# Performance work log

Hardware: AMD Instinct MI355X
Metric: run time of the kernel (lower is better)

The kernel has to match this reference:

```python
import jax, jax.numpy as jnp
import numpy as np

N_NODES = 100000
IN_CH, HIDDEN, OUT_CH = 128, 64, 40
N_EDGES = 1600000


def gcn_conv(x, row, col, W, b, num_nodes):
    """PyG GCNConv: x' = D^-1/2 (A+I) D^-1/2 (x W) + b, self-loops already in row/col."""
    h = x @ W  # [N, out]
    deg = jax.ops.segment_sum(jnp.ones_like(col, dtype=h.dtype), col, num_segments=num_nodes)
    dinv = jnp.where(deg > 0, jax.lax.rsqrt(deg), 0.0)  # [N]
    norm = dinv[row] * dinv[col]  # [E+N]
    msg = h[row] * norm[:, None]  # gather + scale
    out = jax.ops.segment_sum(msg, col, num_segments=num_nodes)  # scatter-add to targets
    return out + b


def setup_inputs() -> dict:
    key = jax.random.key(0)
    k = jax.random.split(key, 6)
    x = jax.random.normal(k[0], (N_NODES, IN_CH), dtype=jnp.float32)
    ei = jax.random.randint(k[1], (2, N_EDGES), 0, N_NODES, dtype=jnp.int64)
    # Glorot-style init for linear weights, zeros for biases (PyG defaults)
    W1 = jax.random.normal(k[2], (IN_CH, HIDDEN), dtype=jnp.float32) / np.sqrt(IN_CH)
    b1 = jnp.zeros((HIDDEN,), dtype=jnp.float32)
    W2 = jax.random.normal(k[3], (HIDDEN, OUT_CH), dtype=jnp.float32) / np.sqrt(HIDDEN)
    b2 = jnp.zeros((OUT_CH,), dtype=jnp.float32)
    return {"x": x, "ei": ei, "W1": W1, "b1": b1, "W2": W2, "b2": b2}


def reference(x, ei, W1, b1, W2, b2):
    num_nodes = x.shape[0]
    loop = jnp.arange(num_nodes, dtype=ei.dtype)
    row = jnp.concatenate([ei[0], loop])  # sources + self-loops
    col = jnp.concatenate([ei[1], loop])  # targets + self-loops
    h = jax.nn.relu(gcn_conv(x, row, col, W1, b1, num_nodes))
    # dropout(p=0.5) is identity in eval mode (deterministic reference)
    return gcn_conv(h, row, col, W2, b2, num_nodes)
```

## Files before the change

kernel.cpp:

```cpp
#include <hip/hip_runtime.h>
#include <hip/hip_bf16.h>
#include <math.h>

#define IN_CH 128
#define HID 64
#define OUT_CH 40
#define NBUCK 1024
#define NBSHIFT 10
#define CAP2 3125
#define CAPL 2560

typedef const __hip_bfloat16* bf16p;
typedef __attribute__((ext_vector_type(8))) short bf16x8;
typedef __attribute__((ext_vector_type(4))) float f32x4;
typedef __attribute__((ext_vector_type(8))) float f32x8;

__device__ __forceinline__ f32x8 cvt8(bf16x8 v) {
    f32x8 o;
    #pragma unroll
    for (int j = 0; j < 8; ++j) {
        unsigned int bits = ((unsigned int)(unsigned short)v[j]) << 16;
        o[j] = __uint_as_float(bits);
    }
    return o;
}

__device__ __forceinline__ bf16x8 pack8(f32x8 v) {
    bf16x8 o;
    #pragma unroll
    for (int j = 0; j < 8; ++j) {
        __hip_bfloat16 b = __float2bfloat16(v[j]);
        o[j] = *reinterpret_cast<short*>(&b);
    }
    return o;
}

__device__ __forceinline__ int bucket_of(int c, int N, float invNB) {
    int b = (int)((float)c * invNB);
    long long cB = (long long)c << NBSHIFT;
    while ((long long)(b + 1) * N <= cB) ++b;
    while (b > 0 && (long long)b * N > cB) --b;
    return b;
}

__global__ __launch_bounds__(256) void k_detectconv(const void* x, const void* ei,
        int* flags, const void* W1, const void* b1, const void* W2, const void* b2,
        float* wf) {
    __shared__ int s_f32, s_hi;
    if (threadIdx.x == 0) { s_f32 = 0; s_hi = 0; }
    __syncthreads();
    const __hip_bfloat16* xb = (const __hip_bfloat16*)x;
    const int* ii = (const int*)ei;
    int lf = 0, lh = 0;
    for (int i = threadIdx.x; i < 4096; i += 256) {
        float f = __bfloat162float(xb[i]);
        if (!(fabsf(f) <= 1e4f)) lf = 1;
        lh |= ii[2 * i + 1];
    }
    if (lf) atomicOr(&s_f32, 1);
    if (lh) atomicOr(&s_hi, 1);
    __syncthreads();
    const int isF32 = s_f32 ? 1 : 0;
    if (threadIdx.x == 0) {
        flags[0] = isF32;
        flags[1] = (s_hi == 0) ? 1 : 0;
        flags[2] = 0;
    }
    for (int i = threadIdx.x; i < 10856; i += 256) {
        const void* src; int off;
        if (i < 8192)       { src = W1; off = i; }
        else if (i < 8256)  { src = b1; off = i - 8192; }
        else if (i < 10816) { src = W2; off = i - 8256; }
        else                { src = b2; off = i - 10816; }
        wf[i] = isF32 ? ((const float*)src)[off]
                      : __bfloat162float(((bf16p)src)[off]);
    }
}

__global__ __launch_bounds__(512) void k_bin2(const int* ei, const int* flags,
        int* bincnt2, long long* bins2, int E, int N, float invNB) {
    __shared__ int cnt[NBUCK], base[NBUCK];
    for (int i = threadIdx.x; i < NBUCK; i += 512) cnt[i] = 0;
    __syncthreads();
    const int i64 = flags[1];
    const int e0 = blockIdx.x * 4096;
    const int e1 = min(e0 + 4096, E);
    int e = e0 + threadIdx.x;
    for (; e + 3 * 512 < e1; e += 4 * 512) {
        int c0 = i64 ? ei[2 * (E + e)]        : ei[E + e];
        int c1 = i64 ? ei[2 * (E + e + 512)]  : ei[E + e + 512];
        int c2 = i64 ? ei[2 * (E + e + 1024)] : ei[E + e + 1024];
        int c3 = i64 ? ei[2 * (E + e + 1536)] : ei[E + e + 1536];
        atomicAdd(&cnt[bucket_of(c0, N, invNB)], 1);
        atomicAdd(&cnt[bucket_of(c1, N, invNB)], 1);
        atomicAdd(&cnt[bucket_of(c2, N, invNB)], 1);
        atomicAdd(&cnt[bucket_of(c3, N, invNB)], 1);
    }
    for (; e < e1; e += 512) {
        int c = i64 ? ei[2 * (E + e)] : ei[E + e];
        atomicAdd(&cnt[bucket_of(c, N, invNB)], 1);
    }
    __syncthreads();
    for (int i = threadIdx.x; i < NBUCK; i += 512) {
        int v = cnt[i];
        base[i] = v ? atomicAdd(&bincnt2[i], v) : 0;
        cnt[i] = 0;
    }
    __syncthreads();
    for (e = e0 + threadIdx.x; e < e1; e += 512) {
        int r, c;
        if (i64) { r = ei[2 * e]; c = ei[2 * (E + e)]; }
        else     { r = ei[e];     c = ei[E + e]; }
        int b = bucket_of(c, N, invNB);
        int slot = base[b] + atomicAdd(&cnt[b], 1);
        if (slot < CAP2)
            bins2[(size_t)b * CAP2 + slot] = ((long long)r << 32) | (unsigned int)c;
    }
}

__global__ __launch_bounds__(256) void k_csr(const long long* bins2, const int* bincnt2,
        int* rowstart, float* dinv, int* erow, int N) {
    __shared__ long long rc[CAPL];
    __shared__ int sdeg[256], lcur[256], red[256];
    const int s = blockIdx.x;
    const int tid = threadIdx.x;
    int part = 0;
    for (int j = tid; j < s; j += 256) part += min(bincnt2[j], CAPL);
    red[tid] = part;
    __syncthreads();
    for (int o = 128; o > 0; o >>= 1) {
        if (tid < o) red[tid] += red[tid + o];
        __syncthreads();
    }
    const int gb = red[0];
    const int nlo = (int)(((long long)s * N + NBUCK - 1) >> NBSHIFT);
    const int nhi = (int)(((long long)(s + 1) * N + NBUCK - 1) >> NBSHIFT);
    const int width = nhi - nlo;
    const int cnt = min(bincnt2[s], CAPL);

    for (int i = tid; i < cnt; i += 256) rc[i] = bins2[(size_t)s * CAP2 + i];
    sdeg[tid] = 0;
    __syncthreads();
    for (int i = tid; i < cnt; i += 256) {
        int j = (int)(rc[i] & 0xffffffffLL) - nlo;
        if (j >= 0 && j < width) atomicAdd(&sdeg[j], 1);
    }
    __syncthreads();
    int my = sdeg[tid];
    __syncthreads();
    for (int off = 1; off < 256; off <<= 1) {
        int t = (tid >= off) ? sdeg[tid - off] : 0;
        __syncthreads();
        sdeg[tid] += t;
        __syncthreads();
    }
    int excl = sdeg[tid] - my;
    lcur[tid] = excl;
    if (tid < width) {
        rowstart[nlo + tid] = gb + excl;
        dinv[nlo + tid] = rsqrtf((float)my + 1.0f);
    }
    if (s == NBUCK - 1 && tid == 0) rowstart[N] = gb + cnt;
    __syncthreads();
    for (int i = tid; i < cnt; i += 256) {
        long long v = rc[i];
        int j = (int)(v & 0xffffffffLL) - nlo;
        if (j >= 0 && j < width) {
            int pos = atomicAdd(&lcur[j], 1);
            erow[gb + pos] = (int)(v >> 32);
        }
    }
}

__global__ __launch_bounds__(256) void k_gemm1_mfma(const void* x, const float* W1f,
        __hip_bfloat16* h1b, const int* flags, int N) {
    __shared__ __align__(16) unsigned short wT[HID][IN_CH];
    for (int i = threadIdx.x; i < IN_CH * HID; i += 256) {
        int k = i >> 6, c = i & 63;
        __hip_bfloat16 b = __float2bfloat16(W1f[i]);
        wT[c][k] = *reinterpret_cast<unsigned short*>(&b);
    }
    __syncthreads();

    const int isF32 = flags[0];
    const int lane = threadIdx.x & 63;
    const int wid  = threadIdx.x >> 6;
    const int r = lane & 15;
    const int g = lane >> 4;

    bf16x8 bfr[4][4];
    #pragma unroll
    for (int nt = 0; nt < 4; ++nt)
        #pragma unroll
        for (int ks = 0; ks < 4; ++ks)
            bfr[nt][ks] = *(const bf16x8*)&wT[nt * 16 + r][ks * 32 + g * 8];

    const int tiles = (N + 15) >> 4;
    for (int t = blockIdx.x * 4 + wid; t < tiles; t += gridDim.x * 4) {
        const int row0 = t * 16;
        int arow = row0 + r; if (arow >= N) arow = N - 1;
        bf16x8 afr[4];
        if (!isF32) {
            const unsigned short* xr = (const unsigned short*)x + (size_t)arow * IN_CH;
            #pragma unroll
            for (int ks = 0; ks < 4; ++ks)
                afr[ks] = *(const bf16x8*)&xr[ks * 32 + g * 8];
        } else {
            const float* xr = (const float*)x + (size_t)arow * IN_CH;
            #pragma unroll
            for (int ks = 0; ks < 4; ++ks) {
                #pragma unroll
                for (int j = 0; j < 8; ++j) {
                    __hip_bfloat16 b = __float2bfloat16(xr[ks * 32 + g * 8 + j]);
                    afr[ks][j] = *reinterpret_cast<short*>(&b);
                }
            }
        }
        f32x4 acc[4] = {};
        #pragma unroll
        for (int ks = 0; ks < 4; ++ks)
            #pragma unroll
            for (int nt = 0; nt < 4; ++nt)
                acc[nt] = __builtin_amdgcn_mfma_f32_16x16x32_bf16(afr[ks], bfr[nt][ks],
                                                                  acc[nt], 0, 0, 0);
        #pragma unroll
        for (int nt = 0; nt < 4; ++nt) {
            #pragma unroll
            for (int q = 0; q < 4; ++q) {
                int rr = row0 + g * 4 + q;
                if (rr < N)
                    h1b[(size_t)rr * HID + nt * 16 + r] = __float2bfloat16(acc[nt][q]);
            }
        }
    }
}

__global__ __launch_bounds__(256) void k_agg1(const int* rowstart, const int* erow,
        const __hip_bfloat16* h1b, const float* dinv, const float* b1f,
        __hip_bfloat16* g, int N) {
    const int lane = threadIdx.x & 63;
    const int sub = lane >> 3;
    const int co  = lane & 7;
    const f32x4 b1a = *(const f32x4*)&b1f[co * 8];
    const f32x4 b1b = *(const f32x4*)&b1f[co * 8 + 4];
    const int wstride = (gridDim.x * 256) >> 6;
    for (int w = (blockIdx.x * 256 + threadIdx.x) >> 6; w < N; w += wstride) {
        int s0 = __builtin_amdgcn_readfirstlane(rowstart[w]);
        int s1 = __builtin_amdgcn_readfirstlane(rowstart[w + 1]);
        float d = dinv[w];
        bf16x8 sv = *(const bf16x8*)&h1b[(size_t)w * HID + co * 8];
        f32x8 acc = {};
        int i = s0 + sub;
        for (; i + 8 < s1; i += 16) {
            int r0 = erow[i], r1 = erow[i + 8];
            float n0 = dinv[r0] * d, n1 = dinv[r1] * d;
            f32x8 v0 = cvt8(*(const bf16x8*)&h1b[(size_t)r0 * HID + co * 8]);
            f32x8 v1 = cvt8(*(const bf16x8*)&h1b[(size_t)r1 * HID + co * 8]);
            #pragma unroll
            for (int j = 0; j < 8; ++j) {
                acc[j] = fmaf(v0[j], n0, acc[j]);
                acc[j] = fmaf(v1[j], n1, acc[j]);
            }
        }
        if (i < s1) {
            int r0 = erow[i];
            float n0 = dinv[r0] * d;
            f32x8 v0 = cvt8(*(const bf16x8*)&h1b[(size_t)r0 * HID + co * 8]);
            #pragma unroll
            for (int j = 0; j < 8; ++j) acc[j] = fmaf(v0[j], n0, acc[j]);
        }
        #pragma unroll
        for (int j = 0; j < 8; ++j) {
            acc[j] += __shfl_xor(acc[j], 8);
            acc[j] += __shfl_xor(acc[j], 16);
            acc[j] += __shfl_xor(acc[j], 32);
        }
        if (sub == 0) {
            float dd = d * d;
            f32x8 sf = cvt8(sv);
            f32x8 gv;
            #pragma unroll
            for (int j = 0; j < 4; ++j) {
                gv[j]     = fmaxf(fmaf(sf[j], dd, acc[j]) + b1a[j], 0.f);
                gv[j + 4] = fmaxf(fmaf(sf[j + 4], dd, acc[j + 4]) + b1b[j], 0.f);
            }
            *(bf16x8*)&g[(size_t)w * HID + co * 8] = pack8(gv);
        }
    }
}

__global__ __launch_bounds__(256) void k_agg2s(const int* rowstart, const int* erow,
        const __hip_bfloat16* g, const float* dinv, __hip_bfloat16* sbuf, int N) {
    const int lane = threadIdx.x & 63;
    const int sub = lane >> 3;
    const int co  = lane & 7;
    const int wstride = (gridDim.x * 256) >> 6;
    for (int w = (blockIdx.x * 256 + threadIdx.x) >> 6; w < N; w += wstride) {
        int s0 = __builtin_amdgcn_readfirstlane(rowstart[w]);
        int s1 = __builtin_amdgcn_readfirstlane(rowstart[w + 1]);
        float d = dinv[w];
        bf16x8 sv = *(const bf16x8*)&g[(size_t)w * HID + co * 8];
        f32x8 acc = {};
        int i = s0 + sub;
        for (; i + 8 < s1; i += 16) {
            int r0 = erow[i], r1 = erow[i + 8];
            float n0 = dinv[r0] * d, n1 = dinv[r1] * d;
            f32x8 v0 = cvt8(*(const bf16x8*)&g[(size_t)r0 * HID + co * 8]);
            f32x8 v1 = cvt8(*(const bf16x8*)&g[(size_t)r1 * HID + co * 8]);
            #pragma unroll
            for (int j = 0; j < 8; ++j) {
                acc[j] = fmaf(v0[j], n0, acc[j]);
                acc[j] = fmaf(v1[j], n1, acc[j]);
            }
        }
        if (i < s1) {
            int r0 = erow[i];
            float n0 = dinv[r0] * d;
            f32x8 v0 = cvt8(*(const bf16x8*)&g[(size_t)r0 * HID + co * 8]);
            #pragma unroll
            for (int j = 0; j < 8; ++j) acc[j] = fmaf(v0[j], n0, acc[j]);
        }
        #pragma unroll
        for (int j = 0; j < 8; ++j) {
            acc[j] += __shfl_xor(acc[j], 8);
            acc[j] += __shfl_xor(acc[j], 16);
            acc[j] += __shfl_xor(acc[j], 32);
        }
        if (sub == 0) {
            float dd = d * d;
            f32x8 sf = cvt8(sv);
            f32x8 ov;
            #pragma unroll
            for (int j = 0; j < 8; ++j) ov[j] = fmaf(sf[j], dd, acc[j]);
            *(bf16x8*)&sbuf[(size_t)w * HID + co * 8] = pack8(ov);
        }
    }
}

__global__ __launch_bounds__(256) void k_gemm2_mfma(const __hip_bfloat16* sbuf,
        const float* W2f, const float* b2f, float* out, int N) {
    __shared__ __align__(16) unsigned short w2T[48][HID];
    for (int i = threadIdx.x; i < 48 * HID; i += 256) {
        int c = i >> 6, k = i & 63;
        float v = (c < OUT_CH) ? W2f[k * OUT_CH + c] : 0.f;
        __hip_bfloat16 b = __float2bfloat16(v);
        w2T[c][k] = *reinterpret_cast<unsigned short*>(&b);
    }
    __syncthreads();

    const int lane = threadIdx.x & 63;
    const int wid  = threadIdx.x >> 6;
    const int r = lane & 15;
    const int gq = lane >> 4;

    bf16x8 bfr[3][2];
    #pragma unroll
    for (int nt = 0; nt < 3; ++nt)
        #pragma unroll
        for (int ks = 0; ks < 2; ++ks)
            bfr[nt][ks] = *(const bf16x8*)&w2T[nt * 16 + r][ks * 32 + gq * 8];
    float b2v[3];
    #pragma unroll
    for (int nt = 0; nt < 3; ++nt)
        b2v[nt] = (nt * 16 + r < OUT_CH) ? b2f[nt * 16 + r] : 0.f;

    const int tiles = (N + 15) >> 4;
    for (int t = blockIdx.x * 4 + wid; t < tiles; t += gridDim.x * 4) {
        const int row0 = t * 16;
        int arow = row0 + r; if (arow >= N) arow = N - 1;
        const unsigned short* sr = (const unsigned short*)sbuf + (size_t)arow * HID;
        bf16x8 afr[2];
        afr[0] = *(const bf16x8*)&sr[gq * 8];
        afr[1] = *(const bf16x8*)&sr[32 + gq * 8];
        f32x4 acc[3] = {};
        #pragma unroll
        for (int ks = 0; ks < 2; ++ks)
            #pragma unroll
            for (int nt = 0; nt < 3; ++nt)
                acc[nt] = __builtin_amdgcn_mfma_f32_16x16x32_bf16(afr[ks], bfr[nt][ks],
                                                                  acc[nt], 0, 0, 0);
        #pragma unroll
        for (int nt = 0; nt < 3; ++nt) {
            int c = nt * 16 + r;
            #pragma unroll
            for (int q = 0; q < 4; ++q) {
                int rr = row0 + gq * 4 + q;
                if (rr < N && c < OUT_CH)
                    out[(size_t)rr * OUT_CH + c] = acc[nt][q] + b2v[nt];
            }
        }
    }
}

extern "C" void kernel_launch(void* const* d_in, const int* in_sizes, int n_in,
                              void* d_out, int out_size, void* d_ws, size_t ws_size,
                              hipStream_t stream) {
    const void* x  = d_in[0];
    const void* ei = d_in[1];
    const void* W1 = d_in[2];
    const void* b1 = d_in[3];
    const void* W2 = d_in[4];
    const void* b2 = d_in[5];
    const int N = in_sizes[0] / IN_CH;
    const int E = in_sizes[1] / 2;
    const int* eii = (const int*)ei;

    float* ws = (float*)d_ws;
    size_t off = 16;
    int*   flags    = (int*)ws;
    int*   bincnt2  = (int*)ws + off;            off += NBUCK;
    float* dinv     = ws + off;                  off += N;
    float* wf       = ws + off;                  off += 10880;
    int*   rowstart = (int*)ws + off;            off += N + 1;
    off = (off + 255) & ~(size_t)255;
    int*   erow     = (int*)ws + off;            off += E;
    off = (off + 255) & ~(size_t)255;
    __hip_bfloat16* h1b = (__hip_bfloat16*)(ws + off);     off += (size_t)N * HID / 2;
    __hip_bfloat16* g   = (__hip_bfloat16*)(ws + off);     off += (size_t)N * HID / 2;
    __hip_bfloat16* sbuf = h1b;
    long long* bins2 = (long long*)h1b;

    hipMemsetAsync(bincnt2, 0, NBUCK * sizeof(int), stream);

    k_detectconv<<<1, 256, 0, stream>>>(x, ei, flags, W1, b1, W2, b2, wf);

    float invNB = (float)NBUCK / (float)N;
    int nbin = (E + 4095) / 4096;
    k_bin2<<<nbin, 512, 0, stream>>>(eii, flags, bincnt2, bins2, E, N, invNB);
    k_csr<<<NBUCK, 256, 0, stream>>>(bins2, bincnt2, rowstart, dinv, erow, N);

    int tiles = (N + 15) / 16;
    int g1 = (tiles + 7) / 8;
    k_gemm1_mfma<<<g1, 256, 0, stream>>>(x, wf, h1b, flags, N);

    k_agg1<<<4096, 256, 0, stream>>>(rowstart, erow, h1b, dinv, wf + 8192, g, N);
    k_agg2s<<<4096, 256, 0, stream>>>(rowstart, erow, g, dinv, sbuf, N);
    k_gemm2_mfma<<<g1, 256, 0, stream>>>(sbuf, wf + 8256, wf + 10816, (float*)d_out, N);
}
```

Baseline: 269.6 us.

## Merge edge binning and first GEMM into one launch; fold memset into detect kernel

Edge binning and the first MFMA GEMM become a single kernel whose blocks branch on blockIdx, so the two independent stages can run concurrently on the GPU. The bins buffer gets its own workspace region instead of aliasing h1b, and the bucket-counter memset moves into the detect kernel, removing one launch. The f32 input path now uses vectorized 16-byte loads. The cost is a larger workspace footprint and a block size of 256 instead of 512 for the binning blocks.

Result: slower. 279.4 us (+3.6%).

```diff
diff --git a/kernel.cpp b/kernel.cpp
--- a/kernel.cpp
+++ b/kernel.cpp
@@ -45,7 +45,7 @@
 
 __global__ __launch_bounds__(256) void k_detectconv(const void* x, const void* ei,
         int* flags, const void* W1, const void* b1, const void* W2, const void* b2,
-        float* wf) {
+        float* wf, int* bincnt2) {
     __shared__ int s_f32, s_hi;
     if (threadIdx.x == 0) { s_f32 = 0; s_hi = 0; }
     __syncthreads();
@@ -59,6 +59,7 @@
     }
     if (lf) atomicOr(&s_f32, 1);
     if (lh) atomicOr(&s_hi, 1);
+    for (int i = threadIdx.x; i < NBUCK; i += 256) bincnt2[i] = 0;
     __syncthreads();
     const int isF32 = s_f32 ? 1 : 0;
     if (threadIdx.x == 0) {
@@ -77,44 +78,116 @@
     }
 }
 
-__global__ __launch_bounds__(512) void k_bin2(const int* ei, const int* flags,
-        int* bincnt2, long long* bins2, int E, int N, float invNB) {
-    __shared__ int cnt[NBUCK], base[NBUCK];
-    for (int i = threadIdx.x; i < NBUCK; i += 512) cnt[i] = 0;
-    __syncthreads();
-    const int i64 = flags[1];
-    const int e0 = blockIdx.x * 4096;
-    const int e1 = min(e0 + 4096, E);
-    int e = e0 + threadIdx.x;
-    for (; e + 3 * 512 < e1; e += 4 * 512) {
-        int c0 = i64 ? ei[2 * (E + e)]        : ei[E + e];
-        int c1 = i64 ? ei[2 * (E + e + 512)]  : ei[E + e + 512];
-        int c2 = i64 ? ei[2 * (E + e + 1024)] : ei[E + e + 1024];
-        int c3 = i64 ? ei[2 * (E + e + 1536)] : ei[E + e + 1536];
-        atomicAdd(&cnt[bucket_of(c0, N, invNB)], 1);
-        atomicAdd(&cnt[bucket_of(c1, N, invNB)], 1);
-        atomicAdd(&cnt[bucket_of(c2, N, invNB)], 1);
-        atomicAdd(&cnt[bucket_of(c3, N, invNB)], 1);
-    }
-    for (; e < e1; e += 512) {
-        int c = i64 ? ei[2 * (E + e)] : ei[E + e];
-        atomicAdd(&cnt[bucket_of(c, N, invNB)], 1);
-    }
-    __syncthreads();
-    for (int i = threadIdx.x; i < NBUCK; i += 512) {
-        int v = cnt[i];
-        base[i] = v ? atomicAdd(&bincnt2[i], v) : 0;
-        cnt[i] = 0;
-    }
-    __syncthreads();
-    for (e = e0 + threadIdx.x; e < e1; e += 512) {
-        int r, c;
-        if (i64) { r = ei[2 * e]; c = ei[2 * (E + e)]; }
-        else     { r = ei[e];     c = ei[E + e]; }
-        int b = bucket_of(c, N, invNB);
-        int slot = base[b] + atomicAdd(&cnt[b], 1);
-        if (slot < CAP2)
-            bins2[(size_t)b * CAP2 + slot] = ((long long)r << 32) | (unsigned int)c;
+__global__ __launch_bounds__(256) void k_bin_gemm1(const int* ei, const int* flags,
+        int* bincnt2, long long* bins2, int E, int N, float invNB, int nbin,
+        const void* x, const float* W1f, __hip_bfloat16* h1b, int g1) {
+    __shared__ __align__(16) unsigned char smem[16384];
+
+    if (blockIdx.x < nbin) {
+        int* cnt  = (int*)smem;
+        int* base = (int*)(smem + 4096);
+        for (int i = threadIdx.x; i < NBUCK; i += 256) cnt[i] = 0;
+        __syncthreads();
+        const int i64 = flags[1];
+        const int e0 = blockIdx.x * 4096;
+        const int e1 = min(e0 + 4096, E);
+        int e = e0 + threadIdx.x;
+        for (; e + 3 * 256 < e1; e += 4 * 256) {
+            int c0 = i64 ? ei[2 * (E + e)]       : ei[E + e];
+            int c1 = i64 ? ei[2 * (E + e + 256)] : ei[E + e + 256];
+            int c2 = i64 ? ei[2 * (E + e + 512)] : ei[E + e + 512];
+            int c3 = i64 ? ei[2 * (E + e + 768)] : ei[E + e + 768];
+            atomicAdd(&cnt[bucket_of(c0, N, invNB)], 1);
+            atomicAdd(&cnt[bucket_of(c1, N, invNB)], 1);
+            atomicAdd(&cnt[bucket_of(c2, N, invNB)], 1);
+            atomicAdd(&cnt[bucket_of(c3, N, invNB)], 1);
+        }
+        for (; e < e1; e += 256) {
+            int c = i64 ? ei[2 * (E + e)] : ei[E + e];
+            atomicAdd(&cnt[bucket_of(c, N, invNB)], 1);
+        }
+        __syncthreads();
+        for (int i = threadIdx.x; i < NBUCK; i += 256) {
+            int v = cnt[i];
+            base[i] = v ? atomicAdd(&bincnt2[i], v) : 0;
+            cnt[i] = 0;
+        }
+        __syncthreads();
+        for (e = e0 + threadIdx.x; e < e1; e += 256) {
+            int r, c;
+            if (i64) { r = ei[2 * e]; c = ei[2 * (E + e)]; }
+            else     { r = ei[e];     c = ei[E + e]; }
+            int b = bucket_of(c, N, invNB);
+            int slot = base[b] + atomicAdd(&cnt[b], 1);
+            if (slot < CAP2)
+                bins2[(size_t)b * CAP2 + slot] = ((long long)r << 32) | (unsigned int)c;
+        }
+        return;
+    }
+
+    unsigned short (*wT)[IN_CH] = (unsigned short(*)[IN_CH])smem;
+    for (int i = threadIdx.x; i < IN_CH * HID; i += 256) {
+        int k = i >> 6, c = i & 63;
+        __hip_bfloat16 b = __float2bfloat16(W1f[i]);
+        wT[c][k] = *reinterpret_cast<unsigned short*>(&b);
+    }
+    __syncthreads();
+
+    const int isF32 = flags[0];
+    const int lane = threadIdx.x & 63;
+    const int wid  = threadIdx.x >> 6;
+    const int r = lane & 15;
+    const int g = lane >> 4;
+    const int bb = blockIdx.x - nbin;
+
+    bf16x8 bfr[4][4];
+    #pragma unroll
+    for (int nt = 0; nt < 4; ++nt)
+        #pragma unroll
+        for (int ks = 0; ks < 4; ++ks)
+            bfr[nt][ks] = *(const bf16x8*)&wT[nt * 16 + r][ks * 32 + g * 8];
+
+    const int tiles = (N + 15) >> 4;
+    for (int t = bb * 4 + wid; t < tiles; t += g1 * 4) {
+        const int row0 = t * 16;
+        int arow = row0 + r; if (arow >= N) arow = N - 1;
+        bf16x8 afr[4];
+        if (!isF32) {
+            const unsigned short* xr = (const unsigned short*)x + (size_t)arow * IN_CH;
+            #pragma unroll
+            for (int ks = 0; ks < 4; ++ks)
+                afr[ks] = *(const bf16x8*)&xr[ks * 32 + g * 8];
+        } else {
+            const float* xr = (const float*)x + (size_t)arow * IN_CH;
+            #pragma unroll
+            for (int ks = 0; ks < 4; ++ks) {
+                f32x4 a0 = *(const f32x4*)&xr[ks * 32 + g * 8];
+                f32x4 a1 = *(const f32x4*)&xr[ks * 32 + g * 8 + 4];
+                #pragma unroll
+                for (int j = 0; j < 4; ++j) {
+                    __hip_bfloat16 b0 = __float2bfloat16(a0[j]);
+                    __hip_bfloat16 b1v = __float2bfloat16(a1[j]);
+                    afr[ks][j]     = *reinterpret_cast<short*>(&b0);
+                    afr[ks][j + 4] = *reinterpret_cast<short*>(&b1v);
+                }
+            }
+        }
+        f32x4 acc[4] = {};
+        #pragma unroll
+        for (int ks = 0; ks < 4; ++ks)
+            #pragma unroll
+            for (int nt = 0; nt < 4; ++nt)
+                acc[nt] = __builtin_amdgcn_mfma_f32_16x16x32_bf16(afr[ks], bfr[nt][ks],
+                                                                  acc[nt], 0, 0, 0);
+        #pragma unroll
+        for (int nt = 0; nt < 4; ++nt) {
+            #pragma unroll
+            for (int q = 0; q < 4; ++q) {
+                int rr = row0 + g * 4 + q;
+                if (rr < N)
+                    h1b[(size_t)rr * HID + nt * 16 + r] = __float2bfloat16(acc[nt][q]);
+            }
+        }
     }
 }
 
@@ -168,69 +241,6 @@
         if (j >= 0 && j < width) {
             int pos = atomicAdd(&lcur[j], 1);
             erow[gb + pos] = (int)(v >> 32);
-        }
-    }
-}
-
-__global__ __launch_bounds__(256) void k_gemm1_mfma(const void* x, const float* W1f,
-        __hip_bfloat16* h1b, const int* flags, int N) {
-    __shared__ __align__(16) unsigned short wT[HID][IN_CH];
-    for (int i = threadIdx.x; i < IN_CH * HID; i += 256) {
-        int k = i >> 6, c = i & 63;
-        __hip_bfloat16 b = __float2bfloat16(W1f[i]);
-        wT[c][k] = *reinterpret_cast<unsigned short*>(&b);
-    }
-    __syncthreads();
-
-    const int isF32 = flags[0];
-    const int lane = threadIdx.x & 63;
-    const int wid  = threadIdx.x >> 6;
-    const int r = lane & 15;
-    const int g = lane >> 4;
-
-    bf16x8 bfr[4][4];
-    #pragma unroll
-    for (int nt = 0; nt < 4; ++nt)
-        #pragma unroll
-        for (int ks = 0; ks < 4; ++ks)
-            bfr[nt][ks] = *(const bf16x8*)&wT[nt * 16 + r][ks * 32 + g * 8];
-
-    const int tiles = (N + 15) >> 4;
-    for (int t = blockIdx.x * 4 + wid; t < tiles; t += gridDim.x * 4) {
-        const int row0 = t * 16;
-        int arow = row0 + r; if (arow >= N) arow = N - 1;
-        bf16x8 afr[4];
-        if (!isF32) {
-            const unsigned short* xr = (const unsigned short*)x + (size_t)arow * IN_CH;
-            #pragma unroll
-            for (int ks = 0; ks < 4; ++ks)
-                afr[ks] = *(const bf16x8*)&xr[ks * 32 + g * 8];
-        } else {
-            const float* xr = (const float*)x + (size_t)arow * IN_CH;
-            #pragma unroll
-            for (int ks = 0; ks < 4; ++ks) {
-                #pragma unroll
-                for (int j = 0; j < 8; ++j) {
-                    __hip_bfloat16 b = __float2bfloat16(xr[ks * 32 + g * 8 + j]);
-                    afr[ks][j] = *reinterpret_cast<short*>(&b);
-                }
-            }
-        }
-        f32x4 acc[4] = {};
-        #pragma unroll
-        for (int ks = 0; ks < 4; ++ks)
-            #pragma unroll
-            for (int nt = 0; nt < 4; ++nt)
-                acc[nt] = __builtin_amdgcn_mfma_f32_16x16x32_bf16(afr[ks], bfr[nt][ks],
-                                                                  acc[nt], 0, 0, 0);
-        #pragma unroll
-        for (int nt = 0; nt < 4; ++nt) {
-            #pragma unroll
-            for (int q = 0; q < 4; ++q) {
-                int rr = row0 + g * 4 + q;
-                if (rr < N)
-                    h1b[(size_t)rr * HID + nt * 16 + r] = __float2bfloat16(acc[nt][q]);
-            }
         }
     }
 }
@@ -417,21 +427,19 @@
     off = (off + 255) & ~(size_t)255;
     __hip_bfloat16* h1b = (__hip_bfloat16*)(ws + off);     off += (size_t)N * HID / 2;
     __hip_bfloat16* g   = (__hip_bfloat16*)(ws + off);     off += (size_t)N * HID / 2;
+    off = (off + 255) & ~(size_t)255;
+    long long* bins2 = (long long*)(ws + off);   off += (size_t)NBUCK * CAP2 * 2;
     __hip_bfloat16* sbuf = h1b;
-    long long* bins2 = (long long*)h1b;
-
-    hipMemsetAsync(bincnt2, 0, NBUCK * sizeof(int), stream);
-
-    k_detectconv<<<1, 256, 0, stream>>>(x, ei, flags, W1, b1, W2, b2, wf);
+
+    k_detectconv<<<1, 256, 0, stream>>>(x, ei, flags, W1, b1, W2, b2, wf, bincnt2);
 
     float invNB = (float)NBUCK / (float)N;
     int nbin = (E + 4095) / 4096;
-    k_bin2<<<nbin, 512, 0, stream>>>(eii, flags, bincnt2, bins2, E, N, invNB);
-    k_csr<<<NBUCK, 256, 0, stream>>>(bins2, bincnt2, rowstart, dinv, erow, N);
-
     int tiles = (N + 15) / 16;
     int g1 = (tiles + 7) / 8;
-    k_gemm1_mfma<<<g1, 256, 0, stream>>>(x, wf, h1b, flags, N);
+    k_bin_gemm1<<<nbin + g1, 256, 0, stream>>>(eii, flags, bincnt2, bins2, E, N,
+                                               invNB, nbin, x, wf, h1b, g1);
+    k_csr<<<NBUCK, 256, 0, stream>>>(bins2, bincnt2, rowstart, dinv, erow, N);
 
     k_agg1<<<4096, 256, 0, stream>>>(rowstart, erow, h1b, dinv, wf + 8192, g, N);
     k_agg2s<<<4096, 256, 0, stream>>>(rowstart, erow, g, dinv, sbuf, N);
```
